# Kernel tuning notes

Measured on AMD Instinct MI355X. Metric: run time of the kernel, lower is better.

The kernel has to match this reference:

```python
import jax, jax.numpy as jnp
import numpy as np

SEQ_LEN, BATCH, T = 128, 32, 32
START, END = 30, 31  # start_tag / end_tag from init_kwargs


def setup_inputs() -> dict:
    key = jax.random.key(0)
    k1, k2 = jax.random.split(key)
    scores = jax.random.normal(k1, (SEQ_LEN, BATCH, T, T, T), dtype=jnp.float32)
    target = jax.random.randint(k2, (SEQ_LEN, BATCH, 1), 0, T ** 3, dtype=jnp.int64)
    mask = jnp.ones((SEQ_LEN, BATCH), dtype=bool)
    return {"scores": scores, "target": target, "mask": mask}


def reference(scores, target, mask):
    seq_len, bat = scores.shape[0], scores.shape[1]

    # gold-path energy: gather flattened tag-triple score at each step, masked sum
    flat = scores.reshape(seq_len, bat, -1)                  # (S, B, T^3)
    tg = jnp.take_along_axis(flat, target, axis=2)[..., 0]   # (S, B)
    tg_energy = jnp.sum(jnp.where(mask, tg, jnp.zeros((), tg.dtype)))

    # init partition over (prev_prev=START fixed out) -> (B, T, T) over (prev, cur)
    p1 = scores[0, :, START, START, :]                       # (B, T)
    partition = p1[:, :, None] + scores[1, :, START, :, :]   # (B, T, T)

    # forward-algorithm recurrence: logsumexp out oldest tag each step
    def step(part, inp):
        s_t, m_t = inp                                       # (B,T,T,T), (B,)
        cur = s_t + part[:, :, :, None]                      # broadcast over new tag
        cp = jax.nn.logsumexp(cur, axis=1)                   # (B, T, T)
        part = jnp.where(m_t[:, None, None], cp, part)
        return part, None

    partition, _ = jax.lax.scan(step, partition, (scores[2:], mask[2:]))

    z = partition[:, END, END].sum()
    return (z - tg_energy) / bat  # average_batch=True
```

## Files before the change

### kernel.cpp

```cpp
#include <hip/hip_runtime.h>
#include <hip/hip_bf16.h>
#include <math.h>

#define SEQ_LEN 128
#define BATCH   32
#define T       32
#define TT      (T*T)
#define TTT     (T*T*T)
#define START   30
#define END     31

#define LOG2E   1.44269504088896f
#define OFF4    5.77078016355587f

typedef unsigned long long u64;

__device__ __forceinline__ u64 pt_pack(int tag, float v) {
    union { float f; unsigned int u; } c; c.f = v;
    return ((u64)(unsigned int)tag << 32) | (u64)c.u;
}
__device__ __forceinline__ float pt_val(u64 w) {
    union { unsigned int u; float f; } c; c.u = (unsigned int)w; return c.f;
}
__device__ __forceinline__ int pt_tag(u64 w) { return (int)(w >> 32); }

__device__ __forceinline__ u64 ald64(const u64* p) {
    return __hip_atomic_load(p, __ATOMIC_RELAXED, __HIP_MEMORY_SCOPE_AGENT);
}
__device__ __forceinline__ void ast64(u64* p, u64 v) {
    __hip_atomic_store(p, v, __ATOMIC_RELAXED, __HIP_MEMORY_SCOPE_AGENT);
}

#define BLOCK_SYNC() do {                                   \
    asm volatile("s_waitcnt lgkmcnt(0)" ::: "memory");      \
    __builtin_amdgcn_sched_barrier(0);                      \
    __builtin_amdgcn_s_barrier();                           \
    __builtin_amdgcn_sched_barrier(0);                      \
} while (0)

__global__ __launch_bounds__(256) void tg_kernel(const float* __restrict__ scores,
                                                 const int*   __restrict__ target,
                                                 const int*   __restrict__ mask,
                                                 float*       __restrict__ ws) {
    int idx = blockIdx.x * 256 + threadIdx.x;
    float v = 0.0f;
    if (mask[idx] != 0) v = scores[(size_t)idx * TTT + target[idx]];
    #pragma unroll
    for (int off = 32; off > 0; off >>= 1) v += __shfl_down(v, off, 64);
    __shared__ float partial[4];
    int wave = threadIdx.x >> 6, lane = threadIdx.x & 63;
    if (lane == 0) partial[wave] = v;
    __syncthreads();
    if (threadIdx.x == 0)
        ws[blockIdx.x] = partial[0] + partial[1] + partial[2] + partial[3];
}

__global__ __launch_bounds__(256) void init_dfb(const float* __restrict__ scores,
                                                u64* __restrict__ ptF,
                                                u64* __restrict__ ptB) {
    const int blk = blockIdx.x, tid = threadIdx.x;
    if (blk < BATCH) {
        const int b = blk;
        u64* pt = ptF + (size_t)b * 2048;
        #pragma unroll
        for (int q = 0; q < 4; ++q) {
            int e = q * 256 + tid;
            int i = e & 31, j = e >> 5;
            float p1 = scores[(size_t)(0*BATCH + b)*TTT + START*TT + START*T + i];
            float s1 = scores[(size_t)(1*BATCH + b)*TTT + START*TT + i*T + j];
            pt[1024 + e] = pt_pack(1, __expf(p1 + s1));
            pt[e]        = 0ULL;
        }
    } else {
        const int b = blk - BATCH;
        u64* pt = ptB + (size_t)b * 2048;
        #pragma unroll
        for (int q = 0; q < 4; ++q) {
            int e = q * 256 + tid;
            float v = (e == END*T + END) ? 1.0f : 0.0f;
            pt[e]        = pt_pack(128, v);
            pt[1024 + e] = 0ULL;
        }
    }
}

__global__ __launch_bounds__(512, 4) void scan_dfb(const float* __restrict__ scores,
                                                   const int*   __restrict__ maskI,
                                                   u64*         __restrict__ ptF,
                                                   u64*         __restrict__ ptB) {
    const int bid   = blockIdx.x;
    const int g     = bid & 7;
    const int chain = bid >> 3;
    const int b     = chain & 31;
    const bool dirB = (chain >> 5) != 0;
    const int tid   = threadIdx.x;
    const int lane  = tid & 63;

    __shared__ float smem[128 * 33];
    __shared__ float pld[128];
    __shared__ float res[128];
    __shared__ int   lmask[SEQ_LEN];

    if (tid < SEQ_LEN) lmask[tid] = maskI[tid * BATCH + b];
    __syncthreads();

    u64* const pt = (dirB ? ptB : ptF) + (size_t)b * 2048;

    const int i0 = tid >> 5;
    const int f  = tid & 31;
    const size_t offA = (size_t)i0 * TT + g * 128 + f * 4;

    const int jjB = (tid & 31) >> 3;
    const int k4  = tid & 7;
    const int oF  = tid >> 2;
    const int s4  = tid & 3;
    const int jjF = oF >> 5;

    float4 SA0, SA1, SB0, SB1;

    auto T_of = [&](int s) { return dirB ? (127 - s) : (2 + s); };

    auto issue = [&](float4& X0, float4& X1, int t) {
        const float* p = scores + ((size_t)t * BATCH + b) * TTT;
        X0 = *(const float4*)(p + offA);
        X1 = *(const float4*)(p + offA + 16 * TT);
    };

    auto addr_of = [&](int o) -> int {
        return dirB ? ((o >> 2) * 32 + 4 * g + (o & 3))
                    : ((o & 31) * 32 + 4 * g + (o >> 5));
    };

    auto step = [&](float4& X0, float4& X1, int t) {
        const bool act   = (lmask[t] != 0);
        const int srcpar = dirB ? ((t + 1) & 1) : ((t - 1) & 1);
        const int tagw   = dirB ? (t + 1) : (t - 1);

        if (!dirB && act) {
            #pragma unroll
            for (int q = 0; q < 4; ++q) smem[(f*4 + q)*33 + i0]        = (&X0.x)[q];
            #pragma unroll
            for (int q = 0; q < 4; ++q) smem[(f*4 + q)*33 + (i0 + 16)] = (&X1.x)[q];
        }

        if (tid < 64) {
            if (act) {
                const u64* src = pt + (size_t)srcpar * 1024 + 128 * g;
                u64 wv0 = 0, wv1 = 0; bool d0 = false, d1 = false;
                while (true) {
                    if (!d0) { wv0 = ald64(src + lane);      d0 = (pt_tag(wv0) == tagw); }
                    if (!d1) { wv1 = ald64(src + 64 + lane); d1 = (pt_tag(wv1) == tagw); }
                    if (__all(d0 && d1)) break;
                }
                pld[lane]      = pt_val(wv0);
                pld[lane + 64] = pt_val(wv1);
            } else {
                const u64* base = pt + (size_t)srcpar * 1024;
                const int o0 = lane, o1 = lane + 64;
                const int a0 = addr_of(o0), a1 = addr_of(o1);
                u64 x0 = 0, x1 = 0; bool d0 = false, d1 = false;
                while (true) {
                    if (!d0) { x0 = ald64(base + a0); d0 = (pt_tag(x0) == tagw); }
                    if (!d1) { x1 = ald64(base + a1); d1 = (pt_tag(x1) == tagw); }
                    if (__all(d0 && d1)) break;
                }
                pld[o0] = pt_val(x0);
                pld[o1] = pt_val(x1);
            }
        }
        BLOCK_SYNC();

        if (act) {
            if (!dirB) {
                float acc = 0.f;
                #pragma unroll
                for (int m = 0; m < 8; ++m) {
                    const int i = s4*8 + m;
                    float E = exp2f(fmaf(smem[oF*33 + i], LOG2E, -OFF4));
                    acc = fmaf(E, pld[jjF*32 + i], acc);
                }
                acc += __shfl_xor(acc, 1, 64);
                acc += __shfl_xor(acc, 2, 64);
                if (s4 == 0) res[oF] = acc;
            } else {
                const float4 Rv = *(const float4*)&pld[jjB*32 + k4*4];
                float acc0, acc1;
                {
                    float e0 = exp2f(fmaf(X0.x, LOG2E, -OFF4));
                    float e1 = exp2f(fmaf(X0.y, LOG2E, -OFF4));
                    float e2 = exp2f(fmaf(X0.z, LOG2E, -OFF4));
                    float e3 = exp2f(fmaf(X0.w, LOG2E, -OFF4));
                    acc0 = fmaf(e3, Rv.w, fmaf(e2, Rv.z, fmaf(e1, Rv.y, e0 * Rv.x)));
                }
                {
                    float e0 = exp2f(fmaf(X1.x, LOG2E, -OFF4));
                    float e1 = exp2f(fmaf(X1.y, LOG2E, -OFF4));
                    float e2 = exp2f(fmaf(X1.z, LOG2E, -OFF4));
                    float e3 = exp2f(fmaf(X1.w, LOG2E, -OFF4));
                    acc1 = fmaf(e3, Rv.w, fmaf(e2, Rv.z, fmaf(e1, Rv.y, e0 * Rv.x)));
                }
                acc0 += __shfl_xor(acc0, 1, 64);
                acc0 += __shfl_xor(acc0, 2, 64);
                acc0 += __shfl_xor(acc0, 4, 64);
                acc1 += __shfl_xor(acc1, 1, 64);
                acc1 += __shfl_xor(acc1, 2, 64);
                acc1 += __shfl_xor(acc1, 4, 64);
                if (k4 == 0) {
                    res[i0*4 + jjB]        = acc0;
                    res[(i0 + 16)*4 + jjB] = acc1;
                }
            }
        }
        BLOCK_SYNC();

        if (tid < 64) {
            const int o0 = lane, o1 = lane + 64;
            const float v0 = act ? res[o0] : pld[o0];
            const float v1 = act ? res[o1] : pld[o1];
            u64* dst = pt + (size_t)(t & 1) * 1024;
            ast64(dst + addr_of(o0), pt_pack(t, v0));
            ast64(dst + addr_of(o1), pt_pack(t, v1));
        }
    };

    issue(SA0, SA1, T_of(0));
    for (int s = 0; s < 63; s += 2) {
        if (s + 1 < 63) issue(SB0, SB1, T_of(s + 1));
        step(SA0, SA1, T_of(s));
        if (s + 1 < 63) {
            if (s + 2 < 63) issue(SA0, SA1, T_of(s + 2));
            step(SB0, SB1, T_of(s + 1));
        }
    }
}

__global__ __launch_bounds__(1024) void finalize_dfb(const float* __restrict__ ws,
                                                     const u64*  __restrict__ ptF,
                                                     const u64*  __restrict__ ptB,
                                                     const int*  __restrict__ mask,
                                                     float*      __restrict__ out) {
    __shared__ float zs[32];
    const int w = threadIdx.x >> 6, lane = threadIdx.x & 63;
    for (int rep = 0; rep < 2; ++rep) {
        const int b = w + rep * 16;
        const u64* qf = ptF + (size_t)b * 2048;
        const u64* rb = ptB + (size_t)b * 2048 + 1024;
        float dot = 0.f;
        #pragma unroll
        for (int e = 0; e < 16; ++e) {
            const int x = lane + 64 * e;
            dot += pt_val(qf[x]) * pt_val(rb[(x & 31) * 32 + (x >> 5)]);
        }
        float cnt = 0.f;
        {
            int t = 2 + lane;
            if (t < SEQ_LEN) cnt += (mask[t*BATCH + b] != 0) ? 1.f : 0.f;
            t += 64;
            if (t < SEQ_LEN) cnt += (mask[t*BATCH + b] != 0) ? 1.f : 0.f;
        }
        #pragma unroll
        for (int off = 32; off > 0; off >>= 1) {
            dot += __shfl_xor(dot, off, 64);
            cnt += __shfl_xor(cnt, off, 64);
        }
        if (lane == 0) zs[b] = 4.0f * cnt + logf(dot);
    }
    __syncthreads();
    if (threadIdx.x == 0) {
        float tg = 0.f, z = 0.f;
        #pragma unroll
        for (int i = 0; i < 16; ++i) tg += ws[i];
        #pragma unroll
        for (int i = 0; i < 32; ++i) z += zs[i];
        out[0] = (z - tg) / (float)BATCH;
    }
}

__global__ __launch_bounds__(1024) void scan_fast(const float* __restrict__ scores,
                                                  const int*   __restrict__ maskI,
                                                  float*       __restrict__ ws) {
    const int b    = blockIdx.x;
    const int tid  = threadIdx.x;
    const int w    = tid >> 6;
    const int lane = tid & 63;
    const int h    = lane >> 4;
    const int jp   = (lane >> 3) & 1;
    const int k4   = lane & 7;
    const int j    = w * 2 + jp;

    __shared__ float Q[2][TT];
    __shared__ int   lmask[SEQ_LEN];
    if (tid < SEQ_LEN) lmask[tid] = maskI[tid * BATCH + b];
    {
        int x = tid >> 5, y = tid & 31;
        float p1 = scores[(size_t)(0*BATCH + b)*TTT + START*TT + START*T + x];
        float s1 = scores[(size_t)(1*BATCH + b)*TTT + START*TT + x*T + y];
        Q[1][x*T + y] = __expf(p1 + s1);
    }
    __syncthreads();
    const int loff = h*8*TT + j*T + k4*4;
    float4 SA[8], SB[8];
    auto issue = [&](float4 (&S)[8], int t) {
        const float* p = scores + ((size_t)t*BATCH + b)*TTT + loff;
        #pragma unroll
        for (int m = 0; m < 8; ++m) S[m] = *(const float4*)(p + m*TT);
    };
    auto process = [&](float4 (&S)[8], int t) {
        const float* qc = Q[(t-1) & 1];
        float*       qn = Q[t & 1];
        #pragma unroll
        for (int m = 0; m < 8; ++m) {
            S[m].x = exp2f(fmaf(S[m].x, LOG2E, -OFF4));
            S[m].y = exp2f(fmaf(S[m].y, LOG2E, -OFF4));
            S[m].z = exp2f(fmaf(S[m].z, LOG2E, -OFF4));
            S[m].w = exp2f(fmaf(S[m].w, LOG2E, -OFF4));
        }
        float4 acc = make_float4(0.f, 0.f, 0.f, 0.f);
        #pragma unroll
        for (int m = 0; m < 8; ++m) {
            float q = qc[(h*8 + m)*T + j];
            acc.x = fmaf(S[m].x, q, acc.x);
            acc.y = fmaf(S[m].y, q, acc.y);
            acc.z = fmaf(S[m].z, q, acc.z);
            acc.w = fmaf(S[m].w, q, acc.w);
        }
        acc.x += __shfl_xor(acc.x, 16, 64); acc.y += __shfl_xor(acc.y, 16, 64);
        acc.z += __shfl_xor(acc.z, 16, 64); acc.w += __shfl_xor(acc.w, 16, 64);
        acc.x += __shfl_xor(acc.x, 32, 64); acc.y += __shfl_xor(acc.y, 32, 64);
        acc.z += __shfl_xor(acc.z, 32, 64); acc.w += __shfl_xor(acc.w, 32, 64);
        if (lane < 16) {
            if (lmask[t] != 0) *(float4*)&qn[j*T + k4*4] = acc;
            else               *(float4*)&qn[j*T + k4*4] = *(const float4*)&qc[j*T + k4*4];
        }
        BLOCK_SYNC();
    };
    issue(SA, 2);
    for (int t = 2; t < SEQ_LEN; t += 2) {
        issue(SB, t + 1);
        process(SA, t);
        if (t + 2 < SEQ_LEN) issue(SA, t + 2);
        process(SB, t + 1);
    }
    if (tid == 0) {
        int cnt = 0;
        for (int t = 2; t < SEQ_LEN; ++t) cnt += (lmask[t] != 0);
        ws[16 + b] = 4.0f * (float)cnt + logf(Q[1][END*T + END]);
    }
}

__global__ void finalize_simple(const float* __restrict__ ws, float* __restrict__ out) {
    if (threadIdx.x == 0) {
        float tg = 0.f, z = 0.f;
        #pragma unroll
        for (int i = 0; i < 16; ++i) tg += ws[i];
        #pragma unroll
        for (int i = 0; i < 32; ++i) z += ws[16 + i];
        out[0] = (z - tg) / (float)BATCH;
    }
}

extern "C" void kernel_launch(void* const* d_in, const int* in_sizes, int n_in,
                              void* d_out, int out_size, void* d_ws, size_t ws_size,
                              hipStream_t stream) {
    const float* scores = (const float*)d_in[0];
    const int*   target = (const int*)d_in[1];
    const int*   mask   = (const int*)d_in[2];
    float* out = (float*)d_out;
    float* ws  = (float*)d_ws;
    u64*   ptF = (u64*)((char*)d_ws + 1024);
    u64*   ptB = ptF + (size_t)BATCH * 2048;
    const size_t need = 1024 + (size_t)2 * BATCH * 2048 * sizeof(u64);

    tg_kernel<<<16, 256, 0, stream>>>(scores, target, mask, ws);
    if (ws_size >= need) {
        init_dfb<<<2*BATCH, 256, 0, stream>>>(scores, ptF, ptB);
        scan_dfb<<<512, 512, 0, stream>>>(scores, mask, ptF, ptB);
        finalize_dfb<<<1, 1024, 0, stream>>>(ws, ptF, ptB, mask, out);
    } else {
        scan_fast<<<BATCH, 1024, 0, stream>>>(scores, mask, ws);
        finalize_simple<<<1, 64, 0, stream>>>(ws, out);
    }
}
```

Before: 187.7 us.

## Process two timesteps per cross-block exchange in the bidirectional forward scan

The scan is restructured so that each of the 8 cooperating blocks per chain handles two timesteps per round. Intermediate results stay in shared memory, and the global tagged-value handshake happens only once per pair. This halves the number of inter-block polling and publish rounds, which dominate the latency of the serial recurrence. In exchange it adds more complex index mapping, extra shared-memory tiles and a second phase per round, with separate handling of masked steps. The fallback kernel's barrier is also replaced with an explicit lgkmcnt wait plus s_barrier.

```diff
diff --git a/kernel.cpp b/kernel.cpp
--- a/kernel.cpp
+++ b/kernel.cpp
@@ -12,6 +12,9 @@
 
 #define LOG2E   1.44269504088896f
 #define OFF4    5.77078016355587f
+
+#define SSTR 33
+#define TSTR 36
 
 typedef unsigned long long u64;
 
@@ -55,7 +58,7 @@
         ws[blockIdx.x] = partial[0] + partial[1] + partial[2] + partial[3];
 }
 
-__global__ __launch_bounds__(256) void init_dfb(const float* __restrict__ scores,
+__global__ __launch_bounds__(256) void init_qfb(const float* __restrict__ scores,
                                                 u64* __restrict__ ptF,
                                                 u64* __restrict__ ptB) {
     const int blk = blockIdx.x, tid = threadIdx.x;
@@ -65,11 +68,11 @@
         #pragma unroll
         for (int q = 0; q < 4; ++q) {
             int e = q * 256 + tid;
-            int i = e & 31, j = e >> 5;
+            int i = e >> 5, j = e & 31;
             float p1 = scores[(size_t)(0*BATCH + b)*TTT + START*TT + START*T + i];
             float s1 = scores[(size_t)(1*BATCH + b)*TTT + START*TT + i*T + j];
-            pt[1024 + e] = pt_pack(1, __expf(p1 + s1));
-            pt[e]        = 0ULL;
+            pt[e]        = pt_pack(0, __expf(p1 + s1));
+            pt[1024 + e] = 0ULL;
         }
     } else {
         const int b = blk - BATCH;
@@ -77,14 +80,13 @@
         #pragma unroll
         for (int q = 0; q < 4; ++q) {
             int e = q * 256 + tid;
-            float v = (e == END*T + END) ? 1.0f : 0.0f;
-            pt[e]        = pt_pack(128, v);
+            pt[e]        = pt_pack(0, (e == END*T + END) ? 1.0f : 0.0f);
             pt[1024 + e] = 0ULL;
         }
     }
 }
 
-__global__ __launch_bounds__(512, 4) void scan_dfb(const float* __restrict__ scores,
+__global__ __launch_bounds__(512, 4) void scan_qfb(const float* __restrict__ scores,
                                                    const int*   __restrict__ maskI,
                                                    u64*         __restrict__ ptF,
                                                    u64*         __restrict__ ptB) {
@@ -94,147 +96,201 @@
     const int b     = chain & 31;
     const bool dirB = (chain >> 5) != 0;
     const int tid   = threadIdx.x;
-    const int lane  = tid & 63;
-
-    __shared__ float smem[128 * 33];
-    __shared__ float pld[128];
-    __shared__ float res[128];
+
+    __shared__ __align__(16) float T1[128 * TSTR];
+    __shared__ __align__(16) float T2[128 * TSTR];
+    __shared__ float Sld[32 * SSTR];
+    __shared__ float Ild[132];
     __shared__ int   lmask[SEQ_LEN];
 
     if (tid < SEQ_LEN) lmask[tid] = maskI[tid * BATCH + b];
     __syncthreads();
 
     u64* const pt = (dirB ? ptB : ptF) + (size_t)b * 2048;
-
-    const int i0 = tid >> 5;
-    const int f  = tid & 31;
-    const size_t offA = (size_t)i0 * TT + g * 128 + f * 4;
-
-    const int jjB = (tid & 31) >> 3;
-    const int k4  = tid & 7;
-    const int oF  = tid >> 2;
-    const int s4  = tid & 3;
-    const int jjF = oF >> 5;
-
-    float4 SA0, SA1, SB0, SB1;
-
-    auto T_of = [&](int s) { return dirB ? (127 - s) : (2 + s); };
-
-    auto issue = [&](float4& X0, float4& X1, int t) {
-        const float* p = scores + ((size_t)t * BATCH + b) * TTT;
-        X0 = *(const float4*)(p + offA);
-        X1 = *(const float4*)(p + offA + 16 * TT);
-    };
-
-    auto addr_of = [&](int o) -> int {
-        return dirB ? ((o >> 2) * 32 + 4 * g + (o & 3))
-                    : ((o & 31) * 32 + 4 * g + (o >> 5));
-    };
-
-    auto step = [&](float4& X0, float4& X1, int t) {
-        const bool act   = (lmask[t] != 0);
-        const int srcpar = dirB ? ((t + 1) & 1) : ((t - 1) & 1);
-        const int tagw   = dirB ? (t + 1) : (t - 1);
-
-        if (!dirB && act) {
-            #pragma unroll
-            for (int q = 0; q < 4; ++q) smem[(f*4 + q)*33 + i0]        = (&X0.x)[q];
-            #pragma unroll
-            for (int q = 0; q < 4; ++q) smem[(f*4 + q)*33 + (i0 + 16)] = (&X1.x)[q];
-        }
-
-        if (tid < 64) {
-            if (act) {
-                const u64* src = pt + (size_t)srcpar * 1024 + 128 * g;
-                u64 wv0 = 0, wv1 = 0; bool d0 = false, d1 = false;
-                while (true) {
-                    if (!d0) { wv0 = ald64(src + lane);      d0 = (pt_tag(wv0) == tagw); }
-                    if (!d1) { wv1 = ald64(src + 64 + lane); d1 = (pt_tag(wv1) == tagw); }
-                    if (__all(d0 && d1)) break;
+    auto sbase = [&](int t) { return scores + ((size_t)t * BATCH + b) * TTT; };
+
+    auto getU = [&](int u, int& tP, int& tQ, int& md) {
+        if (!dirB) {
+            int t0 = 2 + 2*u, t1 = (u < 31) ? 3 + 2*u : -1;
+            int a0 = lmask[t0], a1 = (t1 > 0) ? lmask[t1] : 0;
+            if (a0 && a1)      { md = 2; tP = t0; tQ = t1; }
+            else if (a0 || a1) { md = 1; tP = -1; tQ = a0 ? t0 : t1; }
+            else               { md = 0; tP = -1; tQ = -1; }
+        } else {
+            int th = 127 - 2*u, tl = (u < 31) ? 126 - 2*u : -1;
+            int ah = lmask[th], al = (tl > 0) ? lmask[tl] : 0;
+            if (ah && al)      { md = 2; tP = th; tQ = tl; }
+            else if (ah || al) { md = 1; tP = ah ? th : tl; tQ = -1; }
+            else               { md = 0; tP = -1; tQ = -1; }
+        }
+    };
+
+    size_t offP0, offP1, offQ0, offQ1;
+    if (!dirB) {
+        const int j = tid >> 4, q = tid & 15;
+        offP0 = (size_t)q * TT + j * T + 4*g;
+        offP1 = offP0 + (size_t)16 * TT;
+        offQ0 = (size_t)j * TT + 4*g * T + q * 8;
+        offQ1 = offQ0 + 4;
+    } else {
+        const int jj1 = tid >> 7, e4 = tid & 127;
+        offP0 = (size_t)(4*g + jj1) * TT + e4 * 8;
+        offP1 = offP0 + 4;
+        const int i = tid >> 4, hA = tid & 15, jj2 = hA >> 2, h = hA & 3;
+        offQ0 = (size_t)i * TT + (4*g + jj2) * T + h * 4;
+        offQ1 = offQ0 + 16;
+    }
+
+    float4 P0a{}, P1a{}, Q0a{}, Q1a{}, P0b{}, P1b{}, Q0b{}, Q1b{};
+
+    auto loadRegs = [&](int u, float4& P0, float4& P1, float4& Q0, float4& Q1) {
+        int tP, tQ, md; getU(u, tP, tQ, md);
+        if (!dirB) {
+            if (md == 2) { const float* p = sbase(tP);
+                P0 = *(const float4*)(p + offP0); P1 = *(const float4*)(p + offP1); }
+            if (md >= 1) { const float* p = sbase(tQ);
+                Q0 = *(const float4*)(p + offQ0); Q1 = *(const float4*)(p + offQ1); }
+        } else {
+            if (md >= 1) { const float* p = sbase(tP);
+                P0 = *(const float4*)(p + offP0); P1 = *(const float4*)(p + offP1); }
+            if (md == 2) { const float* p = sbase(tQ);
+                Q0 = *(const float4*)(p + offQ0); Q1 = *(const float4*)(p + offQ1); }
+        }
+    };
+
+    auto scatter = [&](int md, const float4& P0, const float4& P1,
+                       const float4& Q0, const float4& Q1) {
+        if (!dirB) {
+            if (md >= 1) {
+                const int j = tid >> 4, hB = tid & 15, kk = hB >> 2, l0 = 8*(hB & 3);
+                *(float4*)&T1[(j*4 + kk)*TSTR + l0]     = Q0;
+                *(float4*)&T1[(j*4 + kk)*TSTR + l0 + 4] = Q1;
+            }
+        } else {
+            if (md >= 1) {
+                const int jj = tid >> 7, e4 = tid & 127, k = e4 >> 2, l0 = 8*(e4 & 3);
+                *(float4*)&T1[(jj*32 + k)*TSTR + l0]     = P0;
+                *(float4*)&T1[(jj*32 + k)*TSTR + l0 + 4] = P1;
+            }
+            if (md == 2) {
+                const int i = tid >> 4, hA = tid & 15, jj = hA >> 2, h = hA & 3;
+                *(float4*)&T2[(i*4 + jj)*TSTR + h*4]      = Q0;
+                *(float4*)&T2[(i*4 + jj)*TSTR + 16 + h*4] = Q1;
+            }
+        }
+    };
+
+    auto poll = [&](int u) {
+        const u64* src = pt + (size_t)(u & 1) * 1024;
+        const int tagw = u;
+        const int x0 = 2*tid, x1 = 2*tid + 1;
+        u64 w0 = 0, w1 = 0; bool d0 = false, d1 = false;
+        while (true) {
+            if (!d0) { w0 = ald64(src + x0); d0 = (pt_tag(w0) == tagw); }
+            if (!d1) { w1 = ald64(src + x1); d1 = (pt_tag(w1) == tagw); }
+            if (__all(d0 && d1)) break;
+        }
+        Sld[(x0 >> 5)*SSTR + (x0 & 31)] = pt_val(w0);
+        Sld[(x1 >> 5)*SSTR + (x1 & 31)] = pt_val(w1);
+    };
+
+    auto phase1 = [&](int md, const float4& P0, const float4& P1) {
+        if (!dirB) {
+            if (md == 2) {
+                const int j = tid >> 4, q = tid & 15;
+                const float s0 = Sld[q*SSTR + j], s1 = Sld[(q + 16)*SSTR + j];
+                float a0 = exp2f(fmaf(P0.x, LOG2E, -OFF4))*s0 + exp2f(fmaf(P1.x, LOG2E, -OFF4))*s1;
+                float a1 = exp2f(fmaf(P0.y, LOG2E, -OFF4))*s0 + exp2f(fmaf(P1.y, LOG2E, -OFF4))*s1;
+                float a2 = exp2f(fmaf(P0.z, LOG2E, -OFF4))*s0 + exp2f(fmaf(P1.z, LOG2E, -OFF4))*s1;
+                float a3 = exp2f(fmaf(P0.w, LOG2E, -OFF4))*s0 + exp2f(fmaf(P1.w, LOG2E, -OFF4))*s1;
+                #pragma unroll
+                for (int m = 1; m < 16; m <<= 1) {
+                    a0 += __shfl_xor(a0, m, 64); a1 += __shfl_xor(a1, m, 64);
+                    a2 += __shfl_xor(a2, m, 64); a3 += __shfl_xor(a3, m, 64);
                 }
-                pld[lane]      = pt_val(wv0);
-                pld[lane + 64] = pt_val(wv1);
-            } else {
-                const u64* base = pt + (size_t)srcpar * 1024;
-                const int o0 = lane, o1 = lane + 64;
-                const int a0 = addr_of(o0), a1 = addr_of(o1);
-                u64 x0 = 0, x1 = 0; bool d0 = false, d1 = false;
-                while (true) {
-                    if (!d0) { x0 = ald64(base + a0); d0 = (pt_tag(x0) == tagw); }
-                    if (!d1) { x1 = ald64(base + a1); d1 = (pt_tag(x1) == tagw); }
-                    if (__all(d0 && d1)) break;
-                }
-                pld[o0] = pt_val(x0);
-                pld[o1] = pt_val(x1);
-            }
-        }
-        BLOCK_SYNC();
-
-        if (act) {
-            if (!dirB) {
+                if (q == 0) { Ild[j*4+0]=a0; Ild[j*4+1]=a1; Ild[j*4+2]=a2; Ild[j*4+3]=a3; }
+            } else if (md == 1) {
+                if (tid < 128) { const int j = tid >> 2, kk = tid & 3;
+                    Ild[j*4 + kk] = Sld[j*SSTR + 4*g + kk]; }
+            }
+        } else {
+            if (md >= 1) {
+                const int jj = tid >> 7, k = (tid >> 2) & 31, r = tid & 3;
                 float acc = 0.f;
                 #pragma unroll
                 for (int m = 0; m < 8; ++m) {
-                    const int i = s4*8 + m;
-                    float E = exp2f(fmaf(smem[oF*33 + i], LOG2E, -OFF4));
-                    acc = fmaf(E, pld[jjF*32 + i], acc);
+                    const int l = r + 4*m;
+                    acc = fmaf(exp2f(fmaf(T1[(jj*32 + k)*TSTR + l], LOG2E, -OFF4)),
+                               Sld[k*SSTR + l], acc);
                 }
                 acc += __shfl_xor(acc, 1, 64);
                 acc += __shfl_xor(acc, 2, 64);
-                if (s4 == 0) res[oF] = acc;
+                if (r == 0) Ild[jj*SSTR + k] = acc;
+            }
+        }
+    };
+
+    auto phase2pub = [&](int u, int md) {
+        u64* dst = pt + (size_t)((u + 1) & 1) * 1024;
+        const int tg2 = u + 1;
+        if (!dirB) {
+            if (md >= 1) {
+                const int kk = tid >> 7, l = (tid >> 2) & 31, r = tid & 3;
+                float acc = 0.f;
+                #pragma unroll
+                for (int m = 0; m < 8; ++m) {
+                    const int j = r + 4*m;
+                    acc = fmaf(exp2f(fmaf(T1[(j*4 + kk)*TSTR + l], LOG2E, -OFF4)),
+                               Ild[j*4 + kk], acc);
+                }
+                acc += __shfl_xor(acc, 1, 64);
+                acc += __shfl_xor(acc, 2, 64);
+                if (r == 0) ast64(dst + (4*g + kk)*32 + l, pt_pack(tg2, acc));
             } else {
-                const float4 Rv = *(const float4*)&pld[jjB*32 + k4*4];
-                float acc0, acc1;
-                {
-                    float e0 = exp2f(fmaf(X0.x, LOG2E, -OFF4));
-                    float e1 = exp2f(fmaf(X0.y, LOG2E, -OFF4));
-                    float e2 = exp2f(fmaf(X0.z, LOG2E, -OFF4));
-                    float e3 = exp2f(fmaf(X0.w, LOG2E, -OFF4));
-                    acc0 = fmaf(e3, Rv.w, fmaf(e2, Rv.z, fmaf(e1, Rv.y, e0 * Rv.x)));
+                if (tid < 128) { const int kk = tid >> 5, l = tid & 31;
+                    ast64(dst + (4*g + kk)*32 + l,
+                          pt_pack(tg2, Sld[(4*g + kk)*SSTR + l])); }
+            }
+        } else {
+            if (md == 2) {
+                const int i = tid >> 4, jj = (tid >> 2) & 3, r = tid & 3;
+                float acc = 0.f;
+                #pragma unroll
+                for (int m = 0; m < 8; ++m) {
+                    const int k = r + 4*m;
+                    acc = fmaf(exp2f(fmaf(T2[(i*4 + jj)*TSTR + k], LOG2E, -OFF4)),
+                               Ild[jj*SSTR + k], acc);
                 }
-                {
-                    float e0 = exp2f(fmaf(X1.x, LOG2E, -OFF4));
-                    float e1 = exp2f(fmaf(X1.y, LOG2E, -OFF4));
-                    float e2 = exp2f(fmaf(X1.z, LOG2E, -OFF4));
-                    float e3 = exp2f(fmaf(X1.w, LOG2E, -OFF4));
-                    acc1 = fmaf(e3, Rv.w, fmaf(e2, Rv.z, fmaf(e1, Rv.y, e0 * Rv.x)));
-                }
-                acc0 += __shfl_xor(acc0, 1, 64);
-                acc0 += __shfl_xor(acc0, 2, 64);
-                acc0 += __shfl_xor(acc0, 4, 64);
-                acc1 += __shfl_xor(acc1, 1, 64);
-                acc1 += __shfl_xor(acc1, 2, 64);
-                acc1 += __shfl_xor(acc1, 4, 64);
-                if (k4 == 0) {
-                    res[i0*4 + jjB]        = acc0;
-                    res[(i0 + 16)*4 + jjB] = acc1;
-                }
-            }
-        }
+                acc += __shfl_xor(acc, 1, 64);
+                acc += __shfl_xor(acc, 2, 64);
+                if (r == 0) ast64(dst + i*32 + 4*g + jj, pt_pack(tg2, acc));
+            } else if (md == 1) {
+                if (tid < 128) { const int jj = tid >> 5, k = tid & 31;
+                    ast64(dst + (4*g + jj)*32 + k, pt_pack(tg2, Ild[jj*SSTR + k])); }
+            } else {
+                if (tid < 128) { const int jj = tid >> 5, k = tid & 31;
+                    ast64(dst + (4*g + jj)*32 + k,
+                          pt_pack(tg2, Sld[(4*g + jj)*SSTR + k])); }
+            }
+        }
+    };
+
+    loadRegs(0, P0a, P1a, Q0a, Q1a);
+    for (int u = 0; u < 32; ++u) {
+        int tP, tQ, md; getU(u, tP, tQ, md);
+        if (u < 31) loadRegs(u + 1, P0b, P1b, Q0b, Q1b);
+        scatter(md, P0a, P1a, Q0a, Q1a);
+        poll(u);
         BLOCK_SYNC();
-
-        if (tid < 64) {
-            const int o0 = lane, o1 = lane + 64;
-            const float v0 = act ? res[o0] : pld[o0];
-            const float v1 = act ? res[o1] : pld[o1];
-            u64* dst = pt + (size_t)(t & 1) * 1024;
-            ast64(dst + addr_of(o0), pt_pack(t, v0));
-            ast64(dst + addr_of(o1), pt_pack(t, v1));
-        }
-    };
-
-    issue(SA0, SA1, T_of(0));
-    for (int s = 0; s < 63; s += 2) {
-        if (s + 1 < 63) issue(SB0, SB1, T_of(s + 1));
-        step(SA0, SA1, T_of(s));
-        if (s + 1 < 63) {
-            if (s + 2 < 63) issue(SA0, SA1, T_of(s + 2));
-            step(SB0, SB1, T_of(s + 1));
-        }
-    }
-}
-
-__global__ __launch_bounds__(1024) void finalize_dfb(const float* __restrict__ ws,
+        phase1(md, P0a, P1a);
+        BLOCK_SYNC();
+        phase2pub(u, md);
+        BLOCK_SYNC();
+        P0a = P0b; P1a = P1b; Q0a = Q0b; Q1a = Q1b;
+    }
+}
+
+__global__ __launch_bounds__(1024) void finalize_qfb(const float* __restrict__ ws,
                                                      const u64*  __restrict__ ptF,
                                                      const u64*  __restrict__ ptB,
                                                      const int*  __restrict__ mask,
@@ -244,12 +300,12 @@
     for (int rep = 0; rep < 2; ++rep) {
         const int b = w + rep * 16;
         const u64* qf = ptF + (size_t)b * 2048;
-        const u64* rb = ptB + (size_t)b * 2048 + 1024;
+        const u64* rb = ptB + (size_t)b * 2048;
         float dot = 0.f;
         #pragma unroll
         for (int e = 0; e < 16; ++e) {
             const int x = lane + 64 * e;
-            dot += pt_val(qf[x]) * pt_val(rb[(x & 31) * 32 + (x >> 5)]);
+            dot += pt_val(qf[x]) * pt_val(rb[x]);
         }
         float cnt = 0.f;
         {
@@ -332,7 +388,8 @@
             if (lmask[t] != 0) *(float4*)&qn[j*T + k4*4] = acc;
             else               *(float4*)&qn[j*T + k4*4] = *(const float4*)&qc[j*T + k4*4];
         }
-        BLOCK_SYNC();
+        asm volatile("s_waitcnt lgkmcnt(0)" ::: "memory");
+        __builtin_amdgcn_s_barrier();
     };
     issue(SA, 2);
     for (int t = 2; t < SEQ_LEN; t += 2) {
@@ -373,9 +430,9 @@
 
     tg_kernel<<<16, 256, 0, stream>>>(scores, target, mask, ws);
     if (ws_size >= need) {
-        init_dfb<<<2*BATCH, 256, 0, stream>>>(scores, ptF, ptB);
-        scan_dfb<<<512, 512, 0, stream>>>(scores, mask, ptF, ptB);
-        finalize_dfb<<<1, 1024, 0, stream>>>(ws, ptF, ptB, mask, out);
+        init_qfb<<<2*BATCH, 256, 0, stream>>>(scores, ptF, ptB);
+        scan_qfb<<<512, 512, 0, stream>>>(scores, mask, ptF, ptB);
+        finalize_qfb<<<1, 1024, 0, stream>>>(ws, ptF, ptB, mask, out);
     } else {
         scan_fast<<<BATCH, 1024, 0, stream>>>(scores, mask, ws);
         finalize_simple<<<1, 64, 0, stream>>>(ws, out);
```

Result: slower. 256.4 us (+36.6%).

## Poll partition state per thread in registers and use triple-buffered exchange

Applied to the files above, without the earlier changes.

Every thread now polls the tagged partition words it needs directly into registers and writes its own result. This removes the staging through shared memory and two of the block barriers per step. The exchange buffer goes from double to triple buffering, which removes the write-after-read hazard without a block-wide sync. The mask becomes a ballot bitmask instead of an LDS array. The forward direction double-buffers the transposed score tile, so there is a single barrier per step. In exchange, each thread issues more polling atomic loads, and the workspace it needs grows by half.

```diff
diff --git a/kernel.cpp b/kernel.cpp
--- a/kernel.cpp
+++ b/kernel.cpp
@@ -30,6 +30,9 @@
 __device__ __forceinline__ void ast64(u64* p, u64 v) {
     __hip_atomic_store(p, v, __ATOMIC_RELAXED, __HIP_MEMORY_SCOPE_AGENT);
 }
+
+#define WAITV0() do { asm volatile("s_waitcnt vmcnt(0)" ::: "memory");  \
+                      __builtin_amdgcn_sched_barrier(0); } while (0)
 
 #define BLOCK_SYNC() do {                                   \
     asm volatile("s_waitcnt lgkmcnt(0)" ::: "memory");      \
@@ -55,13 +58,13 @@
         ws[blockIdx.x] = partial[0] + partial[1] + partial[2] + partial[3];
 }
 
-__global__ __launch_bounds__(256) void init_dfb(const float* __restrict__ scores,
+__global__ __launch_bounds__(256) void init_reg(const float* __restrict__ scores,
                                                 u64* __restrict__ ptF,
                                                 u64* __restrict__ ptB) {
     const int blk = blockIdx.x, tid = threadIdx.x;
     if (blk < BATCH) {
         const int b = blk;
-        u64* pt = ptF + (size_t)b * 2048;
+        u64* pt = ptF + (size_t)b * 3072;
         #pragma unroll
         for (int q = 0; q < 4; ++q) {
             int e = q * 256 + tid;
@@ -70,21 +73,22 @@
             float s1 = scores[(size_t)(1*BATCH + b)*TTT + START*TT + i*T + j];
             pt[1024 + e] = pt_pack(1, __expf(p1 + s1));
             pt[e]        = 0ULL;
+            pt[2048 + e] = 0ULL;
         }
     } else {
         const int b = blk - BATCH;
-        u64* pt = ptB + (size_t)b * 2048;
+        u64* pt = ptB + (size_t)b * 3072;
         #pragma unroll
         for (int q = 0; q < 4; ++q) {
             int e = q * 256 + tid;
-            float v = (e == END*T + END) ? 1.0f : 0.0f;
-            pt[e]        = pt_pack(128, v);
+            pt[2048 + e] = pt_pack(128, (e == END*T + END) ? 1.0f : 0.0f);
+            pt[e]        = 0ULL;
             pt[1024 + e] = 0ULL;
         }
     }
 }
 
-__global__ __launch_bounds__(512, 4) void scan_dfb(const float* __restrict__ scores,
+__global__ __launch_bounds__(512, 4) void scan_reg(const float* __restrict__ scores,
                                                    const int*   __restrict__ maskI,
                                                    u64*         __restrict__ ptF,
                                                    u64*         __restrict__ ptB) {
@@ -96,145 +100,161 @@
     const int tid   = threadIdx.x;
     const int lane  = tid & 63;
 
-    __shared__ float smem[128 * 33];
-    __shared__ float pld[128];
-    __shared__ float res[128];
-    __shared__ int   lmask[SEQ_LEN];
-
-    if (tid < SEQ_LEN) lmask[tid] = maskI[tid * BATCH + b];
-    __syncthreads();
-
-    u64* const pt = (dirB ? ptB : ptF) + (size_t)b * 2048;
+    const u64 mlo = __ballot(maskI[lane * BATCH + b] != 0);
+    const u64 mhi = __ballot(maskI[(64 + lane) * BATCH + b] != 0);
+
+    u64* const pt = (dirB ? ptB : ptF) + (size_t)b * 3072;
+    auto sb     = [&](int t) { return scores + ((size_t)t * BATCH + b) * TTT; };
+    auto act_of = [&](int t) { return (((t < 64) ? (mlo >> t) : (mhi >> (t - 64))) & 1ULL) != 0ULL; };
 
     const int i0 = tid >> 5;
     const int f  = tid & 31;
     const size_t offA = (size_t)i0 * TT + g * 128 + f * 4;
 
-    const int jjB = (tid & 31) >> 3;
-    const int k4  = tid & 7;
-    const int oF  = tid >> 2;
-    const int s4  = tid & 3;
-    const int jjF = oF >> 5;
-
-    float4 SA0, SA1, SB0, SB1;
-
-    auto T_of = [&](int s) { return dirB ? (127 - s) : (2 + s); };
-
-    auto issue = [&](float4& X0, float4& X1, int t) {
-        const float* p = scores + ((size_t)t * BATCH + b) * TTT;
-        X0 = *(const float4*)(p + offA);
-        X1 = *(const float4*)(p + offA + 16 * TT);
-    };
-
-    auto addr_of = [&](int o) -> int {
-        return dirB ? ((o >> 2) * 32 + 4 * g + (o & 3))
-                    : ((o & 31) * 32 + 4 * g + (o >> 5));
-    };
-
-    auto step = [&](float4& X0, float4& X1, int t) {
-        const bool act   = (lmask[t] != 0);
-        const int srcpar = dirB ? ((t + 1) & 1) : ((t - 1) & 1);
-        const int tagw   = dirB ? (t + 1) : (t - 1);
-
-        if (!dirB && act) {
+    if (!dirB) {
+        __shared__ __align__(16) float sm[2][128 * 33];
+        const int oF = tid >> 2, s4 = tid & 3;
+        const int jj = oF >> 5, k = oF & 31;
+        const int jcol = 4 * g + jj;
+        const int ownW = k * 32 + jcol;
+
+        float lastval = 0.f;
+        if (s4 == 0) lastval = pt_val(ald64(pt + 1024 + ownW));
+
+        float4 A0, A1, B0, B1;
+        auto issue = [&](float4& X, float4& Y, int t) {
+            const float* p = sb(t) + offA;
+            X = *(const float4*)p; Y = *(const float4*)(p + 16 * TT);
+        };
+        auto scat = [&](int buf, const float4& X, const float4& Y) {
             #pragma unroll
-            for (int q = 0; q < 4; ++q) smem[(f*4 + q)*33 + i0]        = (&X0.x)[q];
-            #pragma unroll
-            for (int q = 0; q < 4; ++q) smem[(f*4 + q)*33 + (i0 + 16)] = (&X1.x)[q];
-        }
-
-        if (tid < 64) {
+            for (int q = 0; q < 4; ++q) {
+                sm[buf][(f*4 + q)*33 + i0]      = (&X.x)[q];
+                sm[buf][(f*4 + q)*33 + i0 + 16] = (&Y.x)[q];
+            }
+        };
+        auto stepF = [&](int t, int buf) {
+            const bool act = act_of(t);
+            const int tagw = t - 1;
+            const u64* src = pt + (size_t)((t - 1) % 3) * 1024 + jcol * 32 + 8 * s4;
+            u64* dst = pt + (size_t)(t % 3) * 1024;
+            u64 w0, w1, w2, w3, w4, w5, w6, w7;
+            bool d0=false,d1=false,d2=false,d3=false,d4=false,d5=false,d6=false,d7=false;
+            for (;;) {
+                if (!d0) { w0 = ald64(src + 0); d0 = pt_tag(w0) == tagw; }
+                if (!d1) { w1 = ald64(src + 1); d1 = pt_tag(w1) == tagw; }
+                if (!d2) { w2 = ald64(src + 2); d2 = pt_tag(w2) == tagw; }
+                if (!d3) { w3 = ald64(src + 3); d3 = pt_tag(w3) == tagw; }
+                if (!d4) { w4 = ald64(src + 4); d4 = pt_tag(w4) == tagw; }
+                if (!d5) { w5 = ald64(src + 5); d5 = pt_tag(w5) == tagw; }
+                if (!d6) { w6 = ald64(src + 6); d6 = pt_tag(w6) == tagw; }
+                if (!d7) { w7 = ald64(src + 7); d7 = pt_tag(w7) == tagw; }
+                if (__all(d0 && d1 && d2 && d3 && d4 && d5 && d6 && d7)) break;
+            }
             if (act) {
-                const u64* src = pt + (size_t)srcpar * 1024 + 128 * g;
-                u64 wv0 = 0, wv1 = 0; bool d0 = false, d1 = false;
-                while (true) {
-                    if (!d0) { wv0 = ald64(src + lane);      d0 = (pt_tag(wv0) == tagw); }
-                    if (!d1) { wv1 = ald64(src + 64 + lane); d1 = (pt_tag(wv1) == tagw); }
-                    if (__all(d0 && d1)) break;
-                }
-                pld[lane]      = pt_val(wv0);
-                pld[lane + 64] = pt_val(wv1);
-            } else {
-                const u64* base = pt + (size_t)srcpar * 1024;
-                const int o0 = lane, o1 = lane + 64;
-                const int a0 = addr_of(o0), a1 = addr_of(o1);
-                u64 x0 = 0, x1 = 0; bool d0 = false, d1 = false;
-                while (true) {
-                    if (!d0) { x0 = ald64(base + a0); d0 = (pt_tag(x0) == tagw); }
-                    if (!d1) { x1 = ald64(base + a1); d1 = (pt_tag(x1) == tagw); }
-                    if (__all(d0 && d1)) break;
-                }
-                pld[o0] = pt_val(x0);
-                pld[o1] = pt_val(x1);
-            }
-        }
-        BLOCK_SYNC();
-
-        if (act) {
-            if (!dirB) {
+                const float* row = &sm[buf][oF * 33 + 8 * s4];
                 float acc = 0.f;
-                #pragma unroll
-                for (int m = 0; m < 8; ++m) {
-                    const int i = s4*8 + m;
-                    float E = exp2f(fmaf(smem[oF*33 + i], LOG2E, -OFF4));
-                    acc = fmaf(E, pld[jjF*32 + i], acc);
-                }
+                acc = fmaf(exp2f(fmaf(row[0], LOG2E, -OFF4)), pt_val(w0), acc);
+                acc = fmaf(exp2f(fmaf(row[1], LOG2E, -OFF4)), pt_val(w1), acc);
+                acc = fmaf(exp2f(fmaf(row[2], LOG2E, -OFF4)), pt_val(w2), acc);
+                acc = fmaf(exp2f(fmaf(row[3], LOG2E, -OFF4)), pt_val(w3), acc);
+                acc = fmaf(exp2f(fmaf(row[4], LOG2E, -OFF4)), pt_val(w4), acc);
+                acc = fmaf(exp2f(fmaf(row[5], LOG2E, -OFF4)), pt_val(w5), acc);
+                acc = fmaf(exp2f(fmaf(row[6], LOG2E, -OFF4)), pt_val(w6), acc);
+                acc = fmaf(exp2f(fmaf(row[7], LOG2E, -OFF4)), pt_val(w7), acc);
                 acc += __shfl_xor(acc, 1, 64);
                 acc += __shfl_xor(acc, 2, 64);
-                if (s4 == 0) res[oF] = acc;
+                if (s4 == 0) { lastval = acc; ast64(dst + ownW, pt_pack(t, acc)); }
             } else {
-                const float4 Rv = *(const float4*)&pld[jjB*32 + k4*4];
-                float acc0, acc1;
-                {
-                    float e0 = exp2f(fmaf(X0.x, LOG2E, -OFF4));
-                    float e1 = exp2f(fmaf(X0.y, LOG2E, -OFF4));
-                    float e2 = exp2f(fmaf(X0.z, LOG2E, -OFF4));
-                    float e3 = exp2f(fmaf(X0.w, LOG2E, -OFF4));
-                    acc0 = fmaf(e3, Rv.w, fmaf(e2, Rv.z, fmaf(e1, Rv.y, e0 * Rv.x)));
+                WAITV0();
+                if (s4 == 0) ast64(dst + ownW, pt_pack(t, lastval));
+            }
+        };
+
+        issue(A0, A1, 2); issue(B0, B1, 3);
+        scat(0, A0, A1);
+        BLOCK_SYNC();
+        for (int t = 2; t <= 64; t += 2) {
+            if (t + 2 <= 64) issue(A0, A1, t + 2);
+            stepF(t, 0);
+            if (t + 1 > 64) break;
+            scat(1, B0, B1);
+            BLOCK_SYNC();
+            if (t + 3 <= 64) issue(B0, B1, t + 3);
+            stepF(t + 1, 1);
+            scat(0, A0, A1);
+            BLOCK_SYNC();
+        }
+    } else {
+        const int jjB = f >> 3, k4 = f & 7;
+        const int jb = 4 * g + jjB;
+        const int ownW0 = i0 * 32 + jb, ownW1 = (i0 + 16) * 32 + jb;
+
+        float last0 = 0.f, last1 = 0.f;
+        if (k4 == 0) {
+            last0 = pt_val(ald64(pt + 2048 + ownW0));
+            last1 = pt_val(ald64(pt + 2048 + ownW1));
+        }
+
+        float4 A0, A1, B0, B1;
+        auto issue = [&](float4& X, float4& Y, int t) {
+            const float* p = sb(t) + offA;
+            X = *(const float4*)p; Y = *(const float4*)(p + 16 * TT);
+        };
+        auto stepB = [&](int t, const float4& X, const float4& Y) {
+            const bool act = act_of(t);
+            const int tagw = t + 1;
+            const u64* src = pt + (size_t)((t + 1) % 3) * 1024 + jb * 32 + 4 * k4;
+            u64* dst = pt + (size_t)(t % 3) * 1024;
+            u64 w0, w1, w2, w3;
+            bool d0=false,d1=false,d2=false,d3=false;
+            for (;;) {
+                if (!d0) { w0 = ald64(src + 0); d0 = pt_tag(w0) == tagw; }
+                if (!d1) { w1 = ald64(src + 1); d1 = pt_tag(w1) == tagw; }
+                if (!d2) { w2 = ald64(src + 2); d2 = pt_tag(w2) == tagw; }
+                if (!d3) { w3 = ald64(src + 3); d3 = pt_tag(w3) == tagw; }
+                if (__all(d0 && d1 && d2 && d3)) break;
+            }
+            if (act) {
+                const float r0 = pt_val(w0), r1 = pt_val(w1),
+                            r2 = pt_val(w2), r3 = pt_val(w3);
+                float a0 = 0.f, a1 = 0.f;
+                a0 = fmaf(exp2f(fmaf(X.x, LOG2E, -OFF4)), r0, a0);
+                a0 = fmaf(exp2f(fmaf(X.y, LOG2E, -OFF4)), r1, a0);
+                a0 = fmaf(exp2f(fmaf(X.z, LOG2E, -OFF4)), r2, a0);
+                a0 = fmaf(exp2f(fmaf(X.w, LOG2E, -OFF4)), r3, a0);
+                a1 = fmaf(exp2f(fmaf(Y.x, LOG2E, -OFF4)), r0, a1);
+                a1 = fmaf(exp2f(fmaf(Y.y, LOG2E, -OFF4)), r1, a1);
+                a1 = fmaf(exp2f(fmaf(Y.z, LOG2E, -OFF4)), r2, a1);
+                a1 = fmaf(exp2f(fmaf(Y.w, LOG2E, -OFF4)), r3, a1);
+                a0 += __shfl_xor(a0, 1, 64); a0 += __shfl_xor(a0, 2, 64); a0 += __shfl_xor(a0, 4, 64);
+                a1 += __shfl_xor(a1, 1, 64); a1 += __shfl_xor(a1, 2, 64); a1 += __shfl_xor(a1, 4, 64);
+                if (k4 == 0) {
+                    last0 = a0; last1 = a1;
+                    ast64(dst + ownW0, pt_pack(t, a0));
+                    ast64(dst + ownW1, pt_pack(t, a1));
                 }
-                {
-                    float e0 = exp2f(fmaf(X1.x, LOG2E, -OFF4));
-                    float e1 = exp2f(fmaf(X1.y, LOG2E, -OFF4));
-                    float e2 = exp2f(fmaf(X1.z, LOG2E, -OFF4));
-                    float e3 = exp2f(fmaf(X1.w, LOG2E, -OFF4));
-                    acc1 = fmaf(e3, Rv.w, fmaf(e2, Rv.z, fmaf(e1, Rv.y, e0 * Rv.x)));
-                }
-                acc0 += __shfl_xor(acc0, 1, 64);
-                acc0 += __shfl_xor(acc0, 2, 64);
-                acc0 += __shfl_xor(acc0, 4, 64);
-                acc1 += __shfl_xor(acc1, 1, 64);
-                acc1 += __shfl_xor(acc1, 2, 64);
-                acc1 += __shfl_xor(acc1, 4, 64);
+            } else {
+                WAITV0();
                 if (k4 == 0) {
-                    res[i0*4 + jjB]        = acc0;
-                    res[(i0 + 16)*4 + jjB] = acc1;
+                    ast64(dst + ownW0, pt_pack(t, last0));
+                    ast64(dst + ownW1, pt_pack(t, last1));
                 }
             }
-        }
-        BLOCK_SYNC();
-
-        if (tid < 64) {
-            const int o0 = lane, o1 = lane + 64;
-            const float v0 = act ? res[o0] : pld[o0];
-            const float v1 = act ? res[o1] : pld[o1];
-            u64* dst = pt + (size_t)(t & 1) * 1024;
-            ast64(dst + addr_of(o0), pt_pack(t, v0));
-            ast64(dst + addr_of(o1), pt_pack(t, v1));
-        }
-    };
-
-    issue(SA0, SA1, T_of(0));
-    for (int s = 0; s < 63; s += 2) {
-        if (s + 1 < 63) issue(SB0, SB1, T_of(s + 1));
-        step(SA0, SA1, T_of(s));
-        if (s + 1 < 63) {
-            if (s + 2 < 63) issue(SA0, SA1, T_of(s + 2));
-            step(SB0, SB1, T_of(s + 1));
-        }
-    }
-}
-
-__global__ __launch_bounds__(1024) void finalize_dfb(const float* __restrict__ ws,
+        };
+
+        issue(A0, A1, 127); issue(B0, B1, 126);
+        for (int t = 127; t >= 65; t -= 2) {
+            stepB(t, A0, A1);
+            if (t - 2 >= 65) issue(A0, A1, t - 2);
+            if (t - 1 < 65) break;
+            stepB(t - 1, B0, B1);
+            if (t - 3 >= 65) issue(B0, B1, t - 3);
+        }
+    }
+}
+
+__global__ __launch_bounds__(1024) void finalize_reg(const float* __restrict__ ws,
                                                      const u64*  __restrict__ ptF,
                                                      const u64*  __restrict__ ptB,
                                                      const int*  __restrict__ mask,
@@ -243,8 +263,8 @@
     const int w = threadIdx.x >> 6, lane = threadIdx.x & 63;
     for (int rep = 0; rep < 2; ++rep) {
         const int b = w + rep * 16;
-        const u64* qf = ptF + (size_t)b * 2048;
-        const u64* rb = ptB + (size_t)b * 2048 + 1024;
+        const u64* qf = ptF + (size_t)b * 3072 + 1024;
+        const u64* rb = ptB + (size_t)b * 3072 + 2048;
         float dot = 0.f;
         #pragma unroll
         for (int e = 0; e < 16; ++e) {
@@ -368,14 +388,14 @@
     float* out = (float*)d_out;
     float* ws  = (float*)d_ws;
     u64*   ptF = (u64*)((char*)d_ws + 1024);
-    u64*   ptB = ptF + (size_t)BATCH * 2048;
-    const size_t need = 1024 + (size_t)2 * BATCH * 2048 * sizeof(u64);
+    u64*   ptB = ptF + (size_t)BATCH * 3072;
+    const size_t need = 1024 + (size_t)2 * BATCH * 3072 * sizeof(u64);
 
     tg_kernel<<<16, 256, 0, stream>>>(scores, target, mask, ws);
     if (ws_size >= need) {
-        init_dfb<<<2*BATCH, 256, 0, stream>>>(scores, ptF, ptB);
-        scan_dfb<<<512, 512, 0, stream>>>(scores, mask, ptF, ptB);
-        finalize_dfb<<<1, 1024, 0, stream>>>(ws, ptF, ptB, mask, out);
+        init_reg<<<2*BATCH, 256, 0, stream>>>(scores, ptF, ptB);
+        scan_reg<<<512, 512, 0, stream>>>(scores, mask, ptF, ptB);
+        finalize_reg<<<1, 1024, 0, stream>>>(ws, ptF, ptB, mask, out);
     } else {
         scan_fast<<<BATCH, 1024, 0, stream>>>(scores, mask, ws);
         finalize_simple<<<1, 64, 0, stream>>>(ws, out);
```

Measured after the change: 312.8 us. +66.7%, slower.
